# Optimization experiments

Measured on AMD Instinct MI355X. Metric: run time of the kernel, lower is better.

The kernel has to match this reference:

```python
import jax, jax.numpy as jnp
import numpy as np

B, L, E, H = 4, 4096, 1024, 16
D = E // H
MLP = 4096
EPS = 1e-6


def layer_norm(x, g, b):
    mu = jnp.mean(x, -1, keepdims=True)
    v = jnp.mean((x - mu) ** 2, -1, keepdims=True)
    return (x - mu) * jax.lax.rsqrt(v + 1e-5) * g + b


def setup_inputs() -> dict:
    key = jax.random.key(0)
    ks = jax.random.split(key, 16)
    s = 1.0 / np.sqrt(E)
    inp = {
        "x": jax.random.normal(ks[0], (B, L, E), jnp.float32),
        "Wq": jax.random.normal(ks[1], (E, E), jnp.float32) * s,
        "bq": jnp.zeros((E,), jnp.float32),
        "lnq_g": jnp.ones((E,), jnp.float32), "lnq_b": jnp.zeros((E,), jnp.float32),
        "Wk": jax.random.normal(ks[2], (E, E), jnp.float32) * s,
        "bk": jnp.zeros((E,), jnp.float32),
        "lnk_g": jnp.ones((E,), jnp.float32), "lnk_b": jnp.zeros((E,), jnp.float32),
        "Wv": jax.random.normal(ks[3], (E, E), jnp.float32) * s,
        "bv": jnp.zeros((E,), jnp.float32),
        "lnv_g": jnp.ones((E,), jnp.float32), "lnv_b": jnp.zeros((E,), jnp.float32),
        "Wphi_q": jax.random.normal(ks[4], (E, E), jnp.float32) * s,
        "bphi_q": jax.random.normal(ks[5], (E,), jnp.float32) * 0.01,
        "Wphi_k": jax.random.normal(ks[6], (E, E), jnp.float32) * s,
        "bphi_k": jax.random.normal(ks[7], (E,), jnp.float32) * 0.01,
        "lna_g": jnp.ones((E,), jnp.float32), "lna_b": jnp.zeros((E,), jnp.float32),
        "W1": jax.random.normal(ks[8], (E, MLP), jnp.float32) * s,
        "b1": jnp.zeros((MLP,), jnp.float32),
        "W2": jax.random.normal(ks[9], (MLP, E), jnp.float32) * (1.0 / np.sqrt(MLP)),
        "b2": jnp.zeros((E,), jnp.float32),
        "gamma": jnp.float32(0.1),
        "conv_w": jax.random.normal(ks[10], (E, E // H, 5), jnp.float32) * (1.0 / np.sqrt((E // H) * 5)),
        "conv_b": jnp.zeros((E,), jnp.float32),
    }
    return inp


def reference(x, Wq, bq, lnq_g, lnq_b, Wk, bk, lnk_g, lnk_b, Wv, bv, lnv_g, lnv_b,
              Wphi_q, bphi_q, Wphi_k, bphi_k, lna_g, lna_b, W1, b1, W2, b2,
              gamma, conv_w, conv_b):
    Bx, Lq, Ex = x.shape
    Q = layer_norm(x @ Wq + bq, lnq_g, lnq_b)
    K = layer_norm(x @ Wk + bk, lnk_g, lnk_b)
    V = layer_norm(x @ Wv + bv, lnv_g, lnv_b)
    # add_zero_token=True: prepend zero token to K, V
    Z = jnp.zeros((Bx, 1, Ex), x.dtype)
    K = jnp.concatenate([Z, K], axis=1)
    V = jnp.concatenate([Z, V], axis=1)
    # TanhKernel feature maps
    phiQ = jnp.tanh(Q @ Wphi_q + bphi_q) + 1.0
    phiK = jnp.tanh(K @ Wphi_k + bphi_k) + 1.0
    sh = lambda t: t.reshape(Bx, -1, H, D)
    Qh, Kh, Vh, pQ, pK = sh(Q), sh(K), sh(V), sh(phiQ), sh(phiK)
    # RALA rescaling: global query vs keys, softmax over L_K, scaled by L_Q
    qg = jnp.mean(Qh, axis=1, keepdims=True) / np.sqrt(D)          # [B,1,H,D]
    scores = jnp.einsum('bihd,blhd->bihl', qg, Kh)                 # [B,1,H,Lk]
    alpha = jax.nn.softmax(scores, axis=-1) * Lq
    alpha = jnp.transpose(alpha[:, 0], (0, 2, 1))[..., None]       # [B,Lk,H,1]
    pKs = pK * alpha
    K_sum = pKs.sum(axis=1)                                        # [B,H,D]
    KV = jnp.einsum('blhd,blhe->bhde', pKs, Vh)                    # [B,H,D,D]
    num = jnp.einsum('blhd,bhde->blhe', pQ, KV)                    # [B,Lq,H,D]
    den = jnp.einsum('blhd,bhd->blh', pQ, K_sum)[..., None] + EPS
    attn = (num / den).reshape(Bx, Lq, Ex)
    # gated grouped local conv (kernel=5, pad=2, groups=H)
    xt = jnp.transpose(attn, (0, 2, 1))                            # [B,E,L]
    conv = jax.lax.conv_general_dilated(xt, conv_w, (1,), [(2, 2)],
                                        feature_group_count=H)
    local = gamma * (conv + conv_b[None, :, None])
    attn = attn + jnp.transpose(local, (0, 2, 1))
    attn = layer_norm(attn, lna_g, lna_b)
    # Residual MLP, then outer residual with query_source
    h = jax.nn.gelu(attn @ W1 + b1, approximate=False) @ W2 + b2
    return attn + h + x
```

## Files before the change

kernel.cpp:

```cpp
#include <hip/hip_runtime.h>
#include <hip/hip_bf16.h>

#define B_ 4
#define L_ 4096
#define E_ 1024
#define H_ 16
#define D_ 64
#define MLP_ 4096
#define M_ (B_*L_)
#define LK_ (L_+1)

typedef short bf16x8 __attribute__((ext_vector_type(8)));
typedef float f32x4 __attribute__((ext_vector_type(4)));
typedef unsigned short u16;

__device__ __forceinline__ u16 f2bf(float f){
    union { float f; unsigned u; } x; x.f = f;
    unsigned r = x.u + 0x7FFFu + ((x.u >> 16) & 1u);
    return (u16)(r >> 16);
}
__device__ __forceinline__ float bf2f(u16 u){
    union { unsigned u; float f; } x; x.u = ((unsigned)u) << 16;
    return x.f;
}

__global__ __launch_bounds__(256)
void wcvt(const float* __restrict__ in, u16* __restrict__ out, int K, int N)
{
    __shared__ float t[32][33];
    int tid = threadIdx.x;
    int tx = tid & 31, ty = tid >> 5;
    int bk = blockIdx.y, bn = blockIdx.x;
    #pragma unroll
    for (int i=0;i<4;++i)
        t[ty+8*i][tx] = in[(size_t)(bk*32 + ty + 8*i)*N + bn*32 + tx];
    __syncthreads();
    #pragma unroll
    for (int i=0;i<4;++i)
        out[(size_t)(bn*32 + ty + 8*i)*K + bk*32 + tx] = f2bf(t[tx][ty+8*i]);
}

__global__ __launch_bounds__(256)
void xcvt(const float* __restrict__ in, u16* __restrict__ out)
{
    size_t i = ((size_t)blockIdx.x*256 + threadIdx.x)*4;
    float4 v = *(const float4*)(in + i);
    ushort4 o; o.x=f2bf(v.x); o.y=f2bf(v.y); o.z=f2bf(v.z); o.w=f2bf(v.w);
    *(ushort4*)(out + i) = o;
}

template<int EPI>
__global__ __launch_bounds__(256)
void gemm_bf16(const u16* __restrict__ A, const u16* __restrict__ Wt,
               const float* __restrict__ bias, void* __restrict__ Cout,
               int M, int N, int K,
               const float* __restrict__ P1, const float* __restrict__ P2)
{
    __shared__ u16 As[128*64];
    __shared__ u16 Bs[128*64];
    const int tid = threadIdx.x;
    const int bm = blockIdx.y, bn = blockIdx.x;
    const int lane = tid & 63, w = tid >> 6;
    const int wr = w >> 1, wc = w & 1;
    const int row16 = lane & 15, kb = lane >> 4;
    f32x4 acc[4][4] = {};

    for (int kt = 0; kt < K; kt += 64) {
        #pragma unroll
        for (int i = 0; i < 4; ++i) {
            int c = tid + 256*i;
            int row = c >> 3, kc = c & 7;
            uint4 va = *(const uint4*)(A  + (size_t)(bm*128 + row)*K + kt + kc*8);
            uint4 vb = *(const uint4*)(Wt + (size_t)(bn*128 + row)*K + kt + kc*8);
            int off = row*128 + ((kc*16) ^ ((row & 7) << 4));
            *(uint4*)((char*)As + off) = va;
            *(uint4*)((char*)Bs + off) = vb;
        }
        __syncthreads();
        #pragma unroll
        for (int kk = 0; kk < 2; ++kk) {
            bf16x8 af[4], bfr[4];
            #pragma unroll
            for (int mi = 0; mi < 4; ++mi) {
                int r = wr*64 + mi*16 + row16;
                int off = r*128 + ((kk*64 + kb*16) ^ ((row16 & 7) << 4));
                af[mi] = *(const bf16x8*)((const char*)As + off);
            }
            #pragma unroll
            for (int nj = 0; nj < 4; ++nj) {
                int r = wc*64 + nj*16 + row16;
                int off = r*128 + ((kk*64 + kb*16) ^ ((row16 & 7) << 4));
                bfr[nj] = *(const bf16x8*)((const char*)Bs + off);
            }
            #pragma unroll
            for (int mi = 0; mi < 4; ++mi)
                #pragma unroll
                for (int nj = 0; nj < 4; ++nj)
                    acc[mi][nj] = __builtin_amdgcn_mfma_f32_16x16x32_bf16(af[mi], bfr[nj], acc[mi][nj], 0, 0, 0);
        }
        __syncthreads();
    }
    #pragma unroll
    for (int nj = 0; nj < 4; ++nj) {
        int col = bn*128 + wc*64 + nj*16 + row16;
        float bcol = bias[col];
        #pragma unroll
        for (int mi = 0; mi < 4; ++mi) {
            int rbase = bm*128 + wr*64 + mi*16 + kb*4;
            #pragma unroll
            for (int r = 0; r < 4; ++r) {
                int row = rbase + r;
                float v = acc[mi][nj][r] + bcol;
                if (EPI == 1) v = tanhf(v) + 1.0f;
                if (EPI == 2) {
                    int b = row >> 12, l = row & 4095, h = col >> 6;
                    v = (tanhf(v) + 1.0f) * P1[(size_t)(b*16 + h)*LK_ + 1 + l];
                }
                if (EPI == 3) v = 0.5f*v*(1.0f + erff(v*0.70710678118654752f));
                if (EPI == 4) {
                    ((float*)Cout)[(size_t)row*N + col] = v + P1[(size_t)row*N + col] + P2[(size_t)row*N + col];
                } else {
                    ((u16*)Cout)[(size_t)row*N + col] = f2bf(v);
                }
            }
        }
    }
}

__global__ __launch_bounds__(256)
void ln_bf16(u16* __restrict__ x, const float* __restrict__ g, const float* __restrict__ bta)
{
    __shared__ float red[8];
    const int row = blockIdx.x, tid = threadIdx.x;
    u16* p = x + (size_t)row*E_;
    ushort4 raw = *(const ushort4*)(p + tid*4);
    float v[4] = {bf2f(raw.x), bf2f(raw.y), bf2f(raw.z), bf2f(raw.w)};
    float s=0.f, s2=0.f;
    #pragma unroll
    for (int i=0;i<4;++i){ s += v[i]; s2 += v[i]*v[i]; }
    #pragma unroll
    for (int o=32;o;o>>=1){ s += __shfl_xor(s,o); s2 += __shfl_xor(s2,o); }
    int wv = tid >> 6;
    if ((tid & 63) == 0){ red[wv] = s; red[4+wv] = s2; }
    __syncthreads();
    s  = red[0]+red[1]+red[2]+red[3];
    s2 = red[4]+red[5]+red[6]+red[7];
    float mu = s * (1.0f/E_);
    float var = s2 * (1.0f/E_) - mu*mu;
    float rs = rsqrtf(var + 1e-5f);
    ushort4 o4;
    float r0 = (v[0]-mu)*rs*g[tid*4+0] + bta[tid*4+0];
    float r1 = (v[1]-mu)*rs*g[tid*4+1] + bta[tid*4+1];
    float r2 = (v[2]-mu)*rs*g[tid*4+2] + bta[tid*4+2];
    float r3 = (v[3]-mu)*rs*g[tid*4+3] + bta[tid*4+3];
    o4.x=f2bf(r0); o4.y=f2bf(r1); o4.z=f2bf(r2); o4.w=f2bf(r3);
    *(ushort4*)(p + tid*4) = o4;
}

__global__ __launch_bounds__(256)
void ln_dual(const u16* __restrict__ x, const float* __restrict__ g, const float* __restrict__ bta,
             float* __restrict__ of, u16* __restrict__ ob)
{
    __shared__ float red[8];
    const int row = blockIdx.x, tid = threadIdx.x;
    const u16* p = x + (size_t)row*E_;
    ushort4 raw = *(const ushort4*)(p + tid*4);
    float v[4] = {bf2f(raw.x), bf2f(raw.y), bf2f(raw.z), bf2f(raw.w)};
    float s=0.f, s2=0.f;
    #pragma unroll
    for (int i=0;i<4;++i){ s += v[i]; s2 += v[i]*v[i]; }
    #pragma unroll
    for (int o=32;o;o>>=1){ s += __shfl_xor(s,o); s2 += __shfl_xor(s2,o); }
    int wv = tid >> 6;
    if ((tid & 63) == 0){ red[wv] = s; red[4+wv] = s2; }
    __syncthreads();
    s  = red[0]+red[1]+red[2]+red[3];
    s2 = red[4]+red[5]+red[6]+red[7];
    float mu = s * (1.0f/E_);
    float var = s2 * (1.0f/E_) - mu*mu;
    float rs = rsqrtf(var + 1e-5f);
    float4 rf; ushort4 o4;
    rf.x = (v[0]-mu)*rs*g[tid*4+0] + bta[tid*4+0];
    rf.y = (v[1]-mu)*rs*g[tid*4+1] + bta[tid*4+1];
    rf.z = (v[2]-mu)*rs*g[tid*4+2] + bta[tid*4+2];
    rf.w = (v[3]-mu)*rs*g[tid*4+3] + bta[tid*4+3];
    o4.x=f2bf(rf.x); o4.y=f2bf(rf.y); o4.z=f2bf(rf.z); o4.w=f2bf(rf.w);
    *(float4*)(of + (size_t)row*E_ + tid*4) = rf;
    *(ushort4*)(ob + (size_t)row*E_ + tid*4) = o4;
}

__global__ __launch_bounds__(1024)
void qg_partial(const u16* __restrict__ Q, float* __restrict__ qg)
{
    int b = blockIdx.x >> 6;
    int c = blockIdx.x & 63;
    int e = threadIdx.x;
    float s = 0.f;
    const u16* p = Q + ((size_t)b*L_ + c*64)*E_ + e;
    for (int l=0; l<64; ++l) s += bf2f(p[(size_t)l*E_]);
    atomicAdd(&qg[b*E_ + e], s);
}

__global__ __launch_bounds__(256)
void rala_scores(const u16* __restrict__ K, const float* __restrict__ qg,
                 float* __restrict__ scores)
{
    int blk = blockIdx.x;
    int row0 = blk * 64;
    int b = row0 >> 12;
    int tid = threadIdx.x;
    int lane = tid & 63, w = tid >> 6;
    float qr[16];
    const float qscale = 1.0f/(L_ * 8.0f);
    #pragma unroll
    for (int j=0;j<16;++j) qr[j] = qg[b*E_ + lane*16 + j] * qscale;
    for (int it = 0; it < 16; ++it) {
        int r = row0 + w*16 + it;
        const u16* p = K + (size_t)r*E_ + lane*16;
        uint4 a0 = *(const uint4*)(p);
        uint4 a1 = *(const uint4*)(p + 8);
        const u16* u0 = (const u16*)&a0;
        const u16* u1 = (const u16*)&a1;
        float s = 0.f;
        #pragma unroll
        for (int j=0;j<8;++j) s = fmaf(bf2f(u0[j]), qr[j], s);
        #pragma unroll
        for (int j=0;j<8;++j) s = fmaf(bf2f(u1[j]), qr[8+j], s);
        s += __shfl_xor(s, 1);
        s += __shfl_xor(s, 2);
        if ((lane & 3) == 0) {
            int h = lane >> 2;
            int l = r & (L_-1);
            scores[((size_t)(b*H_ + h))*L_ + l] = s;
        }
    }
}

__global__ __launch_bounds__(256)
void rala_softmax(const float* __restrict__ scores, float* __restrict__ alpha)
{
    __shared__ float red[8];
    int bh = blockIdx.x, tid = threadIdx.x;
    const float* sc = scores + (size_t)bh*L_;
    float v[16];
    float mx = 0.f;
    #pragma unroll
    for (int i=0;i<16;++i){ v[i] = sc[tid + i*256]; mx = fmaxf(mx, v[i]); }
    #pragma unroll
    for (int o=32;o;o>>=1) mx = fmaxf(mx, __shfl_xor(mx,o));
    int wv = tid >> 6;
    if ((tid & 63) == 0) red[wv] = mx;
    __syncthreads();
    mx = fmaxf(fmaxf(red[0],red[1]), fmaxf(red[2],red[3]));
    float sum = 0.f;
    #pragma unroll
    for (int i=0;i<16;++i){ v[i] = expf(v[i]-mx); sum += v[i]; }
    #pragma unroll
    for (int o=32;o;o>>=1) sum += __shfl_xor(sum,o);
    __syncthreads();
    if ((tid & 63) == 0) red[4+wv] = sum;
    __syncthreads();
    float Z = red[4]+red[5]+red[6]+red[7] + expf(-mx);
    float scale = (float)L_ / Z;
    float* al = alpha + (size_t)bh*LK_;
    #pragma unroll
    for (int i=0;i<16;++i) al[1 + tid + i*256] = v[i]*scale;
    if (tid==0) al[0] = expf(-mx)*scale;
}

#define NS_ 8
__global__ __launch_bounds__(256)
void kv_partial(const u16* __restrict__ phiKs, const u16* __restrict__ Vb,
                float* __restrict__ KV, float* __restrict__ Ksum)
{
    __shared__ float Ps[64][65];
    __shared__ float Vs[64][65];
    int blk = blockIdx.x;
    int s = blk & (NS_-1);
    int h = (blk >> 3) & 15;
    int b = blk >> 7;
    int tid = threadIdx.x;
    int tx = tid & 15, ty = tid >> 4;
    const size_t bh = (size_t)(b*H_ + h);
    float acc[4][4] = {};
    float ksl = 0.f;
    for (int ch = 0; ch < 8; ++ch) {
        int lbase = s*512 + ch*64;
        #pragma unroll
        for (int i=0;i<16;++i){
            int idx = tid + i*256;
            int r = idx >> 6, c2 = idx & 63;
            size_t g = ((size_t)b*L_ + lbase + r)*E_ + h*64 + c2;
            Ps[r][c2] = bf2f(phiKs[g]);
            Vs[r][c2] = bf2f(Vb[g]);
        }
        __syncthreads();
        #pragma unroll 8
        for (int l=0; l<64; ++l){
            float p[4], vv[4];
            #pragma unroll
            for (int i=0;i<4;++i) p[i] = Ps[l][ty*4+i];
            #pragma unroll
            for (int j=0;j<4;++j) vv[j] = Vs[l][tx*4+j];
            #pragma unroll
            for (int i=0;i<4;++i)
                #pragma unroll
                for (int j=0;j<4;++j)
                    acc[i][j] = fmaf(p[i], vv[j], acc[i][j]);
        }
        if (tid < 64){
            float t = 0.f;
            #pragma unroll 8
            for (int l=0; l<64; ++l) t += Ps[l][tid];
            ksl += t;
        }
        __syncthreads();
    }
    #pragma unroll
    for (int i=0;i<4;++i)
        #pragma unroll
        for (int j=0;j<4;++j)
            atomicAdd(&KV[(bh*D_ + ty*4+i)*D_ + tx*4+j], acc[i][j]);
    if (tid < 64) atomicAdd(&Ksum[bh*D_ + tid], ksl);
}

__global__ void ksum_zero(const float* __restrict__ bphi_k,
                          const float* __restrict__ alpha, float* __restrict__ Ksum)
{
    int bh = blockIdx.x; int h = bh & 15; int d = threadIdx.x;
    float a0 = alpha[(size_t)bh*LK_];
    Ksum[(size_t)bh*D_ + d] += (tanhf(bphi_k[h*D_ + d]) + 1.0f) * a0;
}

__global__ __launch_bounds__(256)
void attn_core(const u16* __restrict__ phiQ, const float* __restrict__ KV,
               const float* __restrict__ Ksum, u16* __restrict__ attn)
{
    __shared__ float KVs[64][65];
    __shared__ float Ps[64][65];
    __shared__ float Ks_[64];
    int gid = blockIdx.x;
    int h = gid & 15; int rchunk = gid >> 4;
    int row0 = rchunk * 64;
    int b = row0 >> 12;
    const size_t bh = (size_t)(b*H_ + h);
    int tid = threadIdx.x;
    int tx = tid & 15, ty = tid >> 4;
    #pragma unroll
    for (int i=0;i<16;++i){
        int idx = tid + i*256;
        int r = idx >> 6, c2 = idx & 63;
        KVs[r][c2] = KV[bh*D_*D_ + r*64 + c2];
        Ps[r][c2]  = bf2f(phiQ[((size_t)row0 + r)*E_ + h*64 + c2]);
    }
    if (tid < 64) Ks_[tid] = Ksum[bh*D_ + tid];
    __syncthreads();
    float num[4][4] = {};
    float den[4] = {};
    for (int d=0; d<64; ++d){
        float kd = Ks_[d];
        float4 kv4 = *(const float4*)&KVs[d][tx*4];
        float kvv[4] = {kv4.x, kv4.y, kv4.z, kv4.w};
        #pragma unroll
        for (int i=0;i<4;++i){
            float q = Ps[ty*4+i][d];
            den[i] = fmaf(q, kd, den[i]);
            #pragma unroll
            for (int j=0;j<4;++j)
                num[i][j] = fmaf(q, kvv[j], num[i][j]);
        }
    }
    #pragma unroll
    for (int i=0;i<4;++i){
        float r = 1.0f / (den[i] + 1e-6f);
        #pragma unroll
        for (int j=0;j<4;++j)
            attn[((size_t)row0 + ty*4 + i)*E_ + h*64 + tx*4 + j] = f2bf(num[i][j] * r);
    }
}

__global__ __launch_bounds__(256)
void conv_residual(const u16* __restrict__ attn, const float* __restrict__ conv_w,
                   const float* __restrict__ conv_b, const float* __restrict__ gamma_p,
                   u16* __restrict__ out)
{
    __shared__ float As_[68][65];
    __shared__ float Ws_[64][81];
    int blk = blockIdx.x;
    int lc = blk & 63; int h = (blk>>6) & 15; int b = blk >> 10;
    int tid = threadIdx.x;
    int tx = tid & 15, ty = tid >> 4;
    for (int i=tid; i<68*64; i+=256){
        int r = i>>6, cc = i&63;
        int l = lc*64 - 2 + r;
        As_[r][cc] = (l>=0 && l<L_) ? bf2f(attn[((size_t)b*L_+l)*E_ + h*D_ + cc]) : 0.f;
    }
    int e0 = tx*4, l0 = ty*4;
    float acc[4][4] = {};
    for (int dc=0; dc<4; ++dc){
        __syncthreads();
        for (int i=tid; i<64*80; i+=256){
            int ee = i/80, rem = i%80;
            Ws_[ee][rem] = conv_w[((size_t)(h*D_+ee))*320 + dc*80 + rem];
        }
        __syncthreads();
        #pragma unroll
        for (int dd=0; dd<16; ++dd){
            #pragma unroll
            for (int t=0; t<5; ++t){
                float wv[4], av[4];
                #pragma unroll
                for (int j=0;j<4;++j) wv[j] = Ws_[e0+j][dd*5+t];
                #pragma unroll
                for (int i=0;i<4;++i) av[i] = As_[l0+i+t][dc*16+dd];
                #pragma unroll
                for (int i=0;i<4;++i)
                    #pragma unroll
                    for (int j=0;j<4;++j)
                        acc[i][j] = fmaf(av[i], wv[j], acc[i][j]);
            }
        }
    }
    float gamma = *gamma_p;
    #pragma unroll
    for (int i=0;i<4;++i){
        int l = lc*64 + l0 + i;
        #pragma unroll
        for (int j=0;j<4;++j){
            int ee = e0 + j;
            float v = As_[l0+i+2][ee] + gamma*(acc[i][j] + conv_b[h*D_+ee]);
            out[((size_t)b*L_+l)*E_ + h*D_ + ee] = f2bf(v);
        }
    }
}

extern "C" void kernel_launch(void* const* d_in, const int* in_sizes, int n_in,
                              void* d_out, int out_size, void* d_ws, size_t ws_size,
                              hipStream_t stream)
{
    const float* x     = (const float*)d_in[0];
    const float* Wq    = (const float*)d_in[1];
    const float* bq    = (const float*)d_in[2];
    const float* lnq_g = (const float*)d_in[3];
    const float* lnq_b = (const float*)d_in[4];
    const float* Wk    = (const float*)d_in[5];
    const float* bk    = (const float*)d_in[6];
    const float* lnk_g = (const float*)d_in[7];
    const float* lnk_b = (const float*)d_in[8];
    const float* Wv    = (const float*)d_in[9];
    const float* bv    = (const float*)d_in[10];
    const float* lnv_g = (const float*)d_in[11];
    const float* lnv_b = (const float*)d_in[12];
    const float* Wphi_q= (const float*)d_in[13];
    const float* bphi_q= (const float*)d_in[14];
    const float* Wphi_k= (const float*)d_in[15];
    const float* bphi_k= (const float*)d_in[16];
    const float* lna_g = (const float*)d_in[17];
    const float* lna_b = (const float*)d_in[18];
    const float* W1    = (const float*)d_in[19];
    const float* b1    = (const float*)d_in[20];
    const float* W2    = (const float*)d_in[21];
    const float* b2    = (const float*)d_in[22];
    const float* gamma = (const float*)d_in[23];
    const float* conv_w= (const float*)d_in[24];
    const float* conv_b= (const float*)d_in[25];
    float* out = (float*)d_out;

    char* base = (char*)d_ws;
    const size_t WT_SQ = (size_t)E_*E_*2;
    const size_t WT_ALL = 5*WT_SQ + 2*(size_t)E_*MLP_*2;
    const size_t BUF = (size_t)M_*E_*2;
    u16* Wqt  = (u16*)base;
    u16* Wkt  = (u16*)(base + 1*WT_SQ);
    u16* Wvt  = (u16*)(base + 2*WT_SQ);
    u16* Wqpt = (u16*)(base + 3*WT_SQ);
    u16* Wkpt = (u16*)(base + 4*WT_SQ);
    u16* W1t  = (u16*)(base + 5*WT_SQ);
    u16* W2t  = (u16*)(base + 5*WT_SQ + (size_t)E_*MLP_*2);
    char* bufs = base + WT_ALL;
    u16* xb = (u16*)(bufs);
    u16* Qb = (u16*)(bufs + 1*BUF);
    u16* Kb = (u16*)(bufs + 2*BUF);
    u16* Vb = (u16*)(bufs + 3*BUF);
    char* small = bufs + 4*BUF;
    float* qg     = (float*)small;
    float* alpha  = qg + B_*E_;
    float* KV     = alpha + (size_t)B_*H_*LK_;
    float* Ksum   = KV + (size_t)B_*H_*D_*D_;
    float* scores = Ksum + (size_t)B_*H_*D_;
    const size_t need = WT_ALL + 4*BUF +
        ((size_t)B_*E_ + (size_t)B_*H_*LK_ + (size_t)B_*H_*D_*D_ + (size_t)B_*H_*D_
         + (size_t)B_*H_*L_)*4;
    if (ws_size < need) return;

    u16* phiKs = xb;
    u16* phiQ  = Vb;
    u16* attn_b  = Kb;
    u16* attn2_b = Qb;
    float* aln_f = (float*)Kb;
    u16* aln_b   = xb;
    u16* h1      = Qb;

    dim3 blk256(256);
    wcvt<<<dim3(32,32),  blk256, 0, stream>>>(Wq, Wqt, E_, E_);
    wcvt<<<dim3(32,32),  blk256, 0, stream>>>(Wk, Wkt, E_, E_);
    wcvt<<<dim3(32,32),  blk256, 0, stream>>>(Wv, Wvt, E_, E_);
    wcvt<<<dim3(32,32),  blk256, 0, stream>>>(Wphi_q, Wqpt, E_, E_);
    wcvt<<<dim3(32,32),  blk256, 0, stream>>>(Wphi_k, Wkpt, E_, E_);
    wcvt<<<dim3(128,32), blk256, 0, stream>>>(W1, W1t, E_, MLP_);
    wcvt<<<dim3(32,128), blk256, 0, stream>>>(W2, W2t, MLP_, E_);
    xcvt<<<M_*E_/1024, blk256, 0, stream>>>(x, xb);
    hipLaunchKernelGGL((gemm_bf16<0>), dim3(8,128), blk256, 0, stream, xb, Wqt, bq, Qb, M_, E_, E_, nullptr, nullptr);
    hipLaunchKernelGGL((gemm_bf16<0>), dim3(8,128), blk256, 0, stream, xb, Wkt, bk, Kb, M_, E_, E_, nullptr, nullptr);
    hipLaunchKernelGGL((gemm_bf16<0>), dim3(8,128), blk256, 0, stream, xb, Wvt, bv, Vb, M_, E_, E_, nullptr, nullptr);
    ln_bf16<<<M_, 256, 0, stream>>>(Qb, lnq_g, lnq_b);
    ln_bf16<<<M_, 256, 0, stream>>>(Kb, lnk_g, lnk_b);
    ln_bf16<<<M_, 256, 0, stream>>>(Vb, lnv_g, lnv_b);
    hipMemsetAsync(qg, 0, B_*E_*sizeof(float), stream);
    qg_partial<<<B_*64, 1024, 0, stream>>>(Qb, qg);
    rala_scores<<<M_/64, 256, 0, stream>>>(Kb, qg, scores);
    rala_softmax<<<B_*H_, 256, 0, stream>>>(scores, alpha);
    hipLaunchKernelGGL((gemm_bf16<2>), dim3(8,128), blk256, 0, stream, Kb, Wkpt, bphi_k, phiKs, M_, E_, E_, alpha, nullptr);
    hipMemsetAsync(KV,   0, (size_t)B_*H_*D_*D_*sizeof(float), stream);
    hipMemsetAsync(Ksum, 0, (size_t)B_*H_*D_*sizeof(float), stream);
    kv_partial<<<B_*H_*NS_, 256, 0, stream>>>(phiKs, Vb, KV, Ksum);
    ksum_zero<<<B_*H_, 64, 0, stream>>>(bphi_k, alpha, Ksum);
    hipLaunchKernelGGL((gemm_bf16<1>), dim3(8,128), blk256, 0, stream, Qb, Wqpt, bphi_q, phiQ, M_, E_, E_, nullptr, nullptr);
    attn_core<<<(M_/64)*H_, 256, 0, stream>>>(phiQ, KV, Ksum, attn_b);
    conv_residual<<<B_*H_*64, 256, 0, stream>>>(attn_b, conv_w, conv_b, gamma, attn2_b);
    ln_dual<<<M_, 256, 0, stream>>>(attn2_b, lna_g, lna_b, aln_f, aln_b);
    for (int c=0; c<4; ++c){
        const u16* Ain   = aln_b + (size_t)c*4096*E_;
        const float* Rf  = aln_f + (size_t)c*4096*E_;
        const float* xin = x     + (size_t)c*4096*E_;
        float* outc = out + (size_t)c*4096*E_;
        hipLaunchKernelGGL((gemm_bf16<3>), dim3(32,32), blk256, 0, stream, Ain, W1t, b1, h1, 4096, MLP_, E_, nullptr, nullptr);
        hipLaunchKernelGGL((gemm_bf16<4>), dim3(8,32),  blk256, 0, stream, h1, W2t, b2, outc, 4096, E_, MLP_, Rf, xin);
    }
}
```

Before: 1.585 ms.

## Load GEMM tiles directly into LDS and restructure grouped conv kernel

The GEMM tile loads now go straight from global memory to LDS through the global_load_lds builtin, with the XOR swizzle applied on the global-address side, so the data no longer passes through VGPRs before the shared-memory store. Separately, the grouped local conv kernel drops the staged shared-memory weight tile. Each thread now owns one output channel and 16 positions, reads its weights straight from global memory and broadcasts activation rows from LDS. Both changes target load and synchronisation overhead. The conv rewrite trades shared-memory staging for per-thread global weight reads and more registers.

```diff
diff --git a/kernel.cpp b/kernel.cpp
--- a/kernel.cpp
+++ b/kernel.cpp
@@ -24,6 +24,12 @@
     return x.f;
 }
 
+__device__ __forceinline__ void gload16(const u16* g, const u16* l){
+    __builtin_amdgcn_global_load_lds(
+        (const __attribute__((address_space(1))) void*)g,
+        (__attribute__((address_space(3))) void*)l, 16, 0, 0);
+}
+
 __global__ __launch_bounds__(256)
 void wcvt(const float* __restrict__ in, u16* __restrict__ out, int K, int N)
 {
@@ -63,18 +69,18 @@
     const int lane = tid & 63, w = tid >> 6;
     const int wr = w >> 1, wc = w & 1;
     const int row16 = lane & 15, kb = lane >> 4;
+    const u16* Abase = A  + (size_t)bm*128*K;
+    const u16* Bbase = Wt + (size_t)bn*128*K;
     f32x4 acc[4][4] = {};
 
     for (int kt = 0; kt < K; kt += 64) {
         #pragma unroll
-        for (int i = 0; i < 4; ++i) {
-            int c = tid + 256*i;
-            int row = c >> 3, kc = c & 7;
-            uint4 va = *(const uint4*)(A  + (size_t)(bm*128 + row)*K + kt + kc*8);
-            uint4 vb = *(const uint4*)(Wt + (size_t)(bn*128 + row)*K + kt + kc*8);
-            int off = row*128 + ((kc*16) ^ ((row & 7) << 4));
-            *(uint4*)((char*)As + off) = va;
-            *(uint4*)((char*)Bs + off) = vb;
+        for (int c4 = 0; c4 < 4; ++c4) {
+            int seg  = c4*32 + w*8;
+            int row  = seg + (lane >> 3);
+            int col8 = (lane & 7) ^ (row & 7);
+            gload16(Abase + (size_t)row*K + kt + col8*8, As + seg*64);
+            gload16(Bbase + (size_t)row*K + kt + col8*8, Bs + seg*64);
         }
         __syncthreads();
         #pragma unroll
@@ -385,52 +391,37 @@
                    u16* __restrict__ out)
 {
     __shared__ float As_[68][65];
-    __shared__ float Ws_[64][81];
     int blk = blockIdx.x;
     int lc = blk & 63; int h = (blk>>6) & 15; int b = blk >> 10;
     int tid = threadIdx.x;
-    int tx = tid & 15, ty = tid >> 4;
+    int e = tid & 63;
+    int lg = tid >> 6;
     for (int i=tid; i<68*64; i+=256){
         int r = i>>6, cc = i&63;
         int l = lc*64 - 2 + r;
         As_[r][cc] = (l>=0 && l<L_) ? bf2f(attn[((size_t)b*L_+l)*E_ + h*D_ + cc]) : 0.f;
     }
-    int e0 = tx*4, l0 = ty*4;
-    float acc[4][4] = {};
-    for (int dc=0; dc<4; ++dc){
-        __syncthreads();
-        for (int i=tid; i<64*80; i+=256){
-            int ee = i/80, rem = i%80;
-            Ws_[ee][rem] = conv_w[((size_t)(h*D_+ee))*320 + dc*80 + rem];
-        }
-        __syncthreads();
-        #pragma unroll
-        for (int dd=0; dd<16; ++dd){
-            #pragma unroll
-            for (int t=0; t<5; ++t){
-                float wv[4], av[4];
-                #pragma unroll
-                for (int j=0;j<4;++j) wv[j] = Ws_[e0+j][dd*5+t];
-                #pragma unroll
-                for (int i=0;i<4;++i) av[i] = As_[l0+i+t][dc*16+dd];
-                #pragma unroll
-                for (int i=0;i<4;++i)
-                    #pragma unroll
-                    for (int j=0;j<4;++j)
-                        acc[i][j] = fmaf(av[i], wv[j], acc[i][j]);
-            }
-        }
+    __syncthreads();
+    float acc[16] = {};
+    const float* wbase = conv_w + ((size_t)(h*D_ + e))*320;
+    for (int d=0; d<64; ++d){
+        float w0 = wbase[d*5+0], w1 = wbase[d*5+1], w2 = wbase[d*5+2],
+              w3 = wbase[d*5+3], w4 = wbase[d*5+4];
+        float a[20];
+        #pragma unroll
+        for (int r=0;r<20;++r) a[r] = As_[lg*16 + r][d];
+        #pragma unroll
+        for (int i=0;i<16;++i)
+            acc[i] = fmaf(a[i+4],w4, fmaf(a[i+3],w3, fmaf(a[i+2],w2,
+                     fmaf(a[i+1],w1, fmaf(a[i+0],w0, acc[i])))));
     }
     float gamma = *gamma_p;
-    #pragma unroll
-    for (int i=0;i<4;++i){
-        int l = lc*64 + l0 + i;
-        #pragma unroll
-        for (int j=0;j<4;++j){
-            int ee = e0 + j;
-            float v = As_[l0+i+2][ee] + gamma*(acc[i][j] + conv_b[h*D_+ee]);
-            out[((size_t)b*L_+l)*E_ + h*D_ + ee] = f2bf(v);
-        }
+    float bc = conv_b[h*D_ + e];
+    #pragma unroll
+    for (int i=0;i<16;++i){
+        int l = lc*64 + lg*16 + i;
+        float v = As_[lg*16 + i + 2][e] + gamma*(acc[i] + bc);
+        out[((size_t)b*L_+l)*E_ + h*D_ + e] = f2bf(v);
     }
 }
 
```

New measurement: 1.642 ms. 1.04x slower.
